# Optimization experiments

Hardware: AMD Instinct MI355X
Metric: run time of the kernel (lower is better)

## Reference

```python
import itertools
import jax, jax.numpy as jnp
import numpy as np

B, N_TOK, C = 256, 196, 512
NUM_HEADS, KEY_DIM, ATTN_RATIO, RESOLUTION = 8, 32, 4.0, 14
D_V = int(ATTN_RATIO * KEY_DIM)        # 128
DH = D_V * NUM_HEADS                   # 1024
H_QKV = DH + 2 * KEY_DIM * NUM_HEADS   # 1536
SCALE = KEY_DIM ** (-0.5)


def _build_bias_idxs(resolution):
    points = list(itertools.product(range(resolution), range(resolution)))
    attention_offsets = {}
    idxs = []
    for p1 in points:
        for p2 in points:
            offset = (abs(p1[0] - p2[0]), abs(p1[1] - p2[1]))
            if offset not in attention_offsets:
                attention_offsets[offset] = len(attention_offsets)
            idxs.append(attention_offsets[offset])
    n = len(points)
    return np.array(idxs, dtype=np.int64).reshape(n, n), len(attention_offsets)


def setup_inputs() -> dict:
    key = jax.random.key(0)
    ks = jax.random.split(key, 6)
    idxs_np, n_offsets = _build_bias_idxs(RESOLUTION)  # (196,196), 196 offsets
    return {
        "x": jax.random.normal(ks[0], (B, N_TOK, C), dtype=jnp.float32),
        "qkv_w": jax.random.normal(ks[1], (H_QKV, C), dtype=jnp.float32) * (C ** -0.5),
        "qkv_b": jax.random.normal(ks[2], (H_QKV,), dtype=jnp.float32) * 0.01,
        "proj_w": jax.random.normal(ks[3], (C, DH), dtype=jnp.float32) * (DH ** -0.5),
        "proj_b": jax.random.normal(ks[4], (C,), dtype=jnp.float32) * 0.01,
        "attention_biases": jax.random.normal(ks[5], (NUM_HEADS, n_offsets), dtype=jnp.float32) * 0.02,
        "bias_idxs": jnp.asarray(idxs_np),
    }


def reference(x, qkv_w, qkv_b, proj_w, proj_b, attention_biases, bias_idxs):
    Bsz, N, _ = x.shape
    # qkv projection: (B, N, H_QKV) -> (B, heads, N, 2*key_dim + d_v)
    qkv = x @ qkv_w.T + qkv_b
    qkv = qkv.reshape(Bsz, N, NUM_HEADS, -1).transpose(0, 2, 1, 3)
    q = qkv[..., :KEY_DIM]
    k = qkv[..., KEY_DIM:2 * KEY_DIM]
    v = qkv[..., 2 * KEY_DIM:]
    # learned relative-position bias gather: (heads, N, N)
    bias = attention_biases[:, bias_idxs]
    attn = jnp.einsum("bhnd,bhmd->bhnm", q, k) * SCALE + bias
    attn = jax.nn.softmax(attn, axis=-1)
    out = jnp.einsum("bhnm,bhmd->bhnd", attn, v)  # (B, heads, N, d_v)
    out = out.transpose(0, 2, 1, 3).reshape(Bsz, N, DH)
    return out @ proj_w.T + proj_b
```

## Files before the change

### kernel.cpp

```cpp
#include <hip/hip_runtime.h>

typedef __attribute__((ext_vector_type(8))) short bf16x8;
typedef __attribute__((ext_vector_type(4))) float f32x4;
typedef unsigned short u16;
typedef unsigned int   u32;

#define NTOK  196
#define NH    8
#define DVDIM 128
#define CDIM  512
#define DH    1024
#define SCALE2 0.25505654708103197f
#define NEG_BIG -1.0e30f
#define LOG2E 1.4426950408889634f
#define VSTRIDE 200
#define RESCALE_THR 8.0f

__device__ __forceinline__ u16 f2bf(float f) {
  u32 u = __builtin_bit_cast(u32, f);
  u32 r = u + 0x7FFFu + ((u >> 16) & 1u);
  return (u16)(r >> 16);
}

__device__ __forceinline__ u32 cvtpk(float lo, float hi) {
  u32 r;
  asm("v_cvt_pk_bf16_f32 %0, %1, %2" : "=v"(r) : "v"(lo), "v"(hi));
  return r;
}

__device__ __forceinline__ void stage16(const void* g, char* lds_wave_base, int lane) {
#if __has_builtin(__builtin_amdgcn_global_load_lds)
  __builtin_amdgcn_global_load_lds(
      (const __attribute__((address_space(1))) unsigned int*)g,
      (__attribute__((address_space(3))) unsigned int*)lds_wave_base, 16, 0, 0);
#else
  *(uint4*)(lds_wave_base + lane * 16) = *(const uint4*)g;
#endif
}

__global__ __launch_bounds__(256)
void cvt_k(const float* __restrict__ s, u16* __restrict__ d, int n8) {
  int i = blockIdx.x * 256 + threadIdx.x;
  if (i < n8) {
    const float4* sp = (const float4*)s + (size_t)i * 2;
    float4 a = sp[0], b = sp[1];
    uint4 o;
    o.x = (u32)f2bf(a.x) | ((u32)f2bf(a.y) << 16);
    o.y = (u32)f2bf(a.z) | ((u32)f2bf(a.w) << 16);
    o.z = (u32)f2bf(b.x) | ((u32)f2bf(b.y) << 16);
    o.w = (u32)f2bf(b.z) | ((u32)f2bf(b.w) << 16);
    ((uint4*)d)[i] = o;
  }
}

__global__ __launch_bounds__(224)
void biasT_k(const float* __restrict__ ab, const int* __restrict__ bidx,
             float* __restrict__ bT) {
  const int m = threadIdx.x, j = blockIdx.x, h = blockIdx.y;
  float v = NEG_BIG;
  if (j < NTOK && m < NTOK) v = ab[h * NTOK + bidx[m * NTOK + j]] * LOG2E;
  bT[((size_t)h * 256 + j) * 224 + m] = v;
}

template<int K, int NB, int EPI>
__global__ __launch_bounds__(256)
void gemm_k(const u16* __restrict__ A, const u16* __restrict__ W,
            const float* __restrict__ bias,
            u16* __restrict__ q, u16* __restrict__ kk, u16* __restrict__ vT,
            float* __restrict__ out)
{
  __shared__ __align__(16) u16 As[128 * 32];
  __shared__ __align__(16) u16 Bs[128 * 32];
  const int tid  = threadIdx.x;
  const int bid  = blockIdx.x;
  const int xcd  = bid & 7, t = bid >> 3;
  const int bn   = t % NB, bm = xcd * 49 + t / NB;
  const int lane = tid & 63, w = tid >> 6;
  const int c16  = lane & 15, quad = lane >> 4;
  const int wm   = (w >> 1) * 64, wn = (w & 1) * 64;
  f32x4 acc[4][4] = {};

  const u16* Ab = A + (size_t)bm * 128 * K;
  const u16* Wb = W + (size_t)bn * 128 * K;
  char* ldsA = (char*)As + w * 1024;
  char* ldsB = (char*)Bs + w * 1024;

  for (int k0 = 0; k0 < K; k0 += 32) {
    #pragma unroll
    for (int p = 0; p < 2; ++p) {
      const int i = p * 256 + tid;
      const int m = i >> 2, kp = (i & 3) * 8;
      stage16(Ab + (size_t)m * K + k0 + kp, ldsA + p * 4096, lane);
      stage16(Wb + (size_t)m * K + k0 + kp, ldsB + p * 4096, lane);
    }
    __syncthreads();
    bf16x8 af[4], bfr[4];
    #pragma unroll
    for (int mi = 0; mi < 4; ++mi)
      af[mi] = *(const bf16x8*)&As[(wm + mi * 16 + c16) * 32 + quad * 8];
    #pragma unroll
    for (int ni = 0; ni < 4; ++ni)
      bfr[ni] = *(const bf16x8*)&Bs[(wn + ni * 16 + c16) * 32 + quad * 8];
    #pragma unroll
    for (int mi = 0; mi < 4; ++mi)
      #pragma unroll
      for (int ni = 0; ni < 4; ++ni)
        acc[mi][ni] = __builtin_amdgcn_mfma_f32_16x16x32_bf16(af[mi], bfr[ni], acc[mi][ni], 0, 0, 0);
    __syncthreads();
  }

  if (EPI == 0) {
    #pragma unroll
    for (int ni = 0; ni < 4; ++ni) {
      const int gn = bn * 128 + wn + ni * 16 + c16;
      const int h = gn / 192, d = gn - h * 192;
      const float bv = bias[gn];
      #pragma unroll
      for (int mi = 0; mi < 4; ++mi) {
        const int gm0 = bm * 128 + wm + mi * 16 + quad * 4;
        const int bb = gm0 / 196, tok0 = gm0 - bb * 196;
        const size_t bhh = (size_t)bb * 8 + h;
        const float v0 = acc[mi][ni][0] + bv, v1 = acc[mi][ni][1] + bv;
        const float v2 = acc[mi][ni][2] + bv, v3 = acc[mi][ni][3] + bv;
        if (d < 64) {
          u16* dst = (d < 32) ? (q  + (bhh * 196 + tok0) * 32 + d)
                              : (kk + (bhh * 196 + tok0) * 32 + (d - 32));
          dst[0] = f2bf(v0); dst[32] = f2bf(v1); dst[64] = f2bf(v2); dst[96] = f2bf(v3);
        } else {
          ushort4 pk = { f2bf(v0), f2bf(v1), f2bf(v2), f2bf(v3) };
          *(ushort4*)&vT[(bhh * 128 + (d - 64)) * VSTRIDE + tok0] = pk;
        }
      }
    }
  } else {
    #pragma unroll
    for (int ni = 0; ni < 4; ++ni) {
      const int gn = bn * 128 + wn + ni * 16 + c16;
      const float bv = bias[gn];
      #pragma unroll
      for (int mi = 0; mi < 4; ++mi) {
        const int gm0 = bm * 128 + wm + mi * 16 + quad * 4;
        #pragma unroll
        for (int r = 0; r < 4; ++r)
          out[(size_t)(gm0 + r) * CDIM + gn] = acc[mi][ni][r] + bv;
      }
    }
  }
}

__global__ __launch_bounds__(256)
void attn_k(const u16* __restrict__ q, const u16* __restrict__ kk,
            const u16* __restrict__ vT, const float* __restrict__ bT,
            u16* __restrict__ Ob)
{
  __shared__ __align__(16) char smem[80896];
  u16* k_lds  = (u16*)smem;
  u16* vt_lds = (u16*)(smem + 20480);
  u16* p_lds  = (u16*)(smem + 71680);

  const int bh = blockIdx.x;
  const int b = bh >> 3, h = bh & 7;
  const int tid = threadIdx.x;
  const int lane = tid & 63, w = tid >> 6;
  const int c16 = lane & 15, quad = lane >> 4;
  const u16* qb = q  + (size_t)bh * (NTOK * 32);
  const u16* kb = kk + (size_t)bh * (NTOK * 32);
  const u16* vb = vT + (size_t)bh * (DVDIM * VSTRIDE);
  const float* bTh = bT + (size_t)h * 256 * 224;
  const f32x4 zf = {0.f, 0.f, 0.f, 0.f};
  u16* pw = p_lds + w * 16 * 72;

  {
    const char* vbb = (const char*)vb;
    for (int c = w; c < 50; c += 4)
      stage16(vbb + c * 1024 + lane * 16, (char*)vt_lds + c * 1024, lane);
  }
  #pragma unroll
  for (int p = 0; p < 4; ++p) {
    const int i = p * 256 + tid;
    const int row = i >> 2, part = (i & 3) * 8;
    const uint4 val = *(const uint4*)(kb + (size_t)min(row, NTOK - 1) * 32 + part);
    *(uint4*)&k_lds[row * 40 + part] = val;
  }
  __syncthreads();
  {
    const int row = tid >> 1, half = tid & 1;
    *(u32*)&vt_lds[row * VSTRIDE + 196 + half * 2] = 0u;
  }
  __syncthreads();

  const int nt_iter = 3 + ((w == (bh & 3)) ? 1 : 0);
  for (int t = 0; t < nt_iter; ++t) {
    const int ti = (t < 3) ? (w + 4 * t) : 12;
    const int tok = min(ti * 16 + c16, NTOK - 1);
    const bf16x8 qf = *(const bf16x8*)(qb + (size_t)tok * 32 + quad * 8);
    const int qg = min(ti * 16 + c16, 223);
    float mx = NEG_BIG, lsum = 0.f;
    f32x4 oacc[8] = {};

    for (int kc = 0; kc < 4; ++kc) {
      f32x4 sc[4];
      __builtin_amdgcn_s_setprio(1);
      #pragma unroll
      for (int nt = 0; nt < 4; ++nt) {
        bf16x8 kf = *(const bf16x8*)&k_lds[(kc * 64 + nt * 16 + c16) * 40 + quad * 8];
        sc[nt] = __builtin_amdgcn_mfma_f32_16x16x32_bf16(kf, qf, zf, 0, 0, 0);
      }
      __builtin_amdgcn_s_setprio(0);

      float ntmx[4];
      #pragma unroll
      for (int nt = 0; nt < 4; ++nt) {
        const float* bp = bTh + (size_t)(kc * 64 + nt * 16 + quad * 4) * 224 + qg;
        #pragma unroll
        for (int r = 0; r < 4; ++r)
          sc[nt][r] = sc[nt][r] * SCALE2 + bp[r * 224];
        ntmx[nt] = fmaxf(fmaxf(sc[nt][0], sc[nt][1]), fmaxf(sc[nt][2], sc[nt][3]));
      }
      const float cmx = fmaxf(fmaxf(ntmx[0], ntmx[1]), fmaxf(ntmx[2], ntmx[3]));

      float alpha = 1.0f;
      if (__ballot(cmx > mx + RESCALE_THR)) {
        float rmx = fmaxf(cmx, __shfl_xor(cmx, 16));
        rmx = fmaxf(rmx, __shfl_xor(rmx, 32));
        const float nmx = fmaxf(mx, rmx);
        alpha = exp2f(mx - nmx);
        mx = nmx;
        float a4[4];
        #pragma unroll
        for (int r = 0; r < 4; ++r) a4[r] = __shfl(alpha, quad * 4 + r);
        #pragma unroll
        for (int nt = 0; nt < 8; ++nt)
          #pragma unroll
          for (int r = 0; r < 4; ++r) oacc[nt][r] *= a4[r];
      }

      const float m = mx;
      float csum = 0.f;
      #pragma unroll
      for (int nt = 0; nt < 4; ++nt) {
        const float p0 = exp2f(sc[nt][0] - m), p1 = exp2f(sc[nt][1] - m);
        const float p2 = exp2f(sc[nt][2] - m), p3 = exp2f(sc[nt][3] - m);
        csum += (p0 + p1) + (p2 + p3);
        uint2 pk;
        pk.x = cvtpk(p0, p1);
        pk.y = cvtpk(p2, p3);
        *(uint2*)&pw[c16 * 72 + nt * 16 + quad * 4] = pk;
      }
      csum += __shfl_xor(csum, 16);
      csum += __shfl_xor(csum, 32);
      lsum = lsum * alpha + csum;

      __builtin_amdgcn_s_setprio(1);
      #pragma unroll
      for (int ks = 0; ks < 2; ++ks) {
        bf16x8 ap = *(const bf16x8*)&pw[c16 * 72 + ks * 32 + quad * 8];
        #pragma unroll
        for (int nt = 0; nt < 8; ++nt) {
          bf16x8 bv = *(const bf16x8*)&vt_lds[(nt * 16 + c16) * VSTRIDE + kc * 64 + ks * 32 + quad * 8];
          oacc[nt] = __builtin_amdgcn_mfma_f32_16x16x32_bf16(ap, bv, oacc[nt], 0, 0, 0);
        }
      }
      __builtin_amdgcn_s_setprio(0);
    }

    float lr[4];
    #pragma unroll
    for (int r = 0; r < 4; ++r) lr[r] = __shfl(lsum, quad * 4 + r);
    #pragma unroll
    for (int r = 0; r < 4; ++r) {
      const int m = ti * 16 + quad * 4 + r;
      if (m < NTOK) {
        const float inv = 1.0f / lr[r];
        #pragma unroll
        for (int nt = 0; nt < 8; ++nt)
          Ob[((size_t)b * NTOK + m) * DH + h * DVDIM + nt * 16 + c16] =
              f2bf(oacc[nt][r] * inv);
      }
    }
  }
}

extern "C" void kernel_launch(void* const* d_in, const int* in_sizes, int n_in,
                              void* d_out, int out_size, void* d_ws, size_t ws_size,
                              hipStream_t stream) {
  const float* x      = (const float*)d_in[0];
  const float* qkv_w  = (const float*)d_in[1];
  const float* qkv_b  = (const float*)d_in[2];
  const float* proj_w = (const float*)d_in[3];
  const float* proj_b = (const float*)d_in[4];
  const float* ab     = (const float*)d_in[5];
  const int*   bidx   = (const int*)d_in[6];
  float* out = (float*)d_out;

  char* p = (char*)d_ws;
  u16*   qw  = (u16*)(p);
  u16*   kw  = (u16*)(p + 25690112);
  u16*   vTw = (u16*)(p + 51380224);
  u16*   w1b = (u16*)(p + 156237824);
  u16*   w3b = (u16*)(p + 157810688);
  float* bT  = (float*)(p + 158859264);
  u16*   xb  = (u16*)(p + 160694272);
  u16*   Ob  = (u16*)(p + 160694272);

  cvt_k<<<12544, 256, 0, stream>>>(x,      xb,  3211264);
  cvt_k<<<  384, 256, 0, stream>>>(qkv_w,  w1b,   98304);
  cvt_k<<<  256, 256, 0, stream>>>(proj_w, w3b,   65536);
  biasT_k<<<dim3(256, 8), 224, 0, stream>>>(ab, bidx, bT);

  gemm_k<512, 12, 0><<<4704, 256, 0, stream>>>(xb, w1b, qkv_b, qw, kw, vTw, nullptr);

  attn_k<<<2048, 256, 0, stream>>>(qw, kw, vTw, bT, Ob);

  gemm_k<1024, 4, 1><<<1568, 256, 0, stream>>>(Ob, w3b, proj_b, nullptr, nullptr, nullptr, out);
}
```

Before: 541.6 us.

## Read V directly from global memory instead of staging it in LDS

The attention kernel no longer copies the transposed V tile into shared memory. The PV MFMA loop now loads V fragments straight from global memory, and zeroing of V's padding columns moves into the QKV projection epilogue. Shared memory per block shrinks from about 80KB to about 25KB, which is meant to allow more resident blocks per CU and remove the staging pass and a barrier. In exchange, each wave re-reads V through the cache hierarchy for every query tile, adding load latency inside the hot loop, and the last head may read slightly past the end of the buffer.

```diff
diff --git a/kernel.cpp b/kernel.cpp
--- a/kernel.cpp
+++ b/kernel.cpp
@@ -128,7 +128,12 @@
           dst[0] = f2bf(v0); dst[32] = f2bf(v1); dst[64] = f2bf(v2); dst[96] = f2bf(v3);
         } else {
           ushort4 pk = { f2bf(v0), f2bf(v1), f2bf(v2), f2bf(v3) };
-          *(ushort4*)&vT[(bhh * 128 + (d - 64)) * VSTRIDE + tok0] = pk;
+          u16* vrow = vT + (bhh * 128 + (d - 64)) * VSTRIDE;
+          *(ushort4*)&vrow[tok0] = pk;
+          if (tok0 == 192) {
+            ushort4 z = {0, 0, 0, 0};
+            *(ushort4*)&vrow[196] = z;
+          }
         }
       }
     }
@@ -153,10 +158,9 @@
             const u16* __restrict__ vT, const float* __restrict__ bT,
             u16* __restrict__ Ob)
 {
-  __shared__ __align__(16) char smem[80896];
-  u16* k_lds  = (u16*)smem;
-  u16* vt_lds = (u16*)(smem + 20480);
-  u16* p_lds  = (u16*)(smem + 71680);
+  __shared__ __align__(16) char smem[25216];
+  u16* k_lds = (u16*)smem;
+  u16* p_lds = (u16*)(smem + 16000);
 
   const int bh = blockIdx.x;
   const int b = bh >> 3, h = bh & 7;
@@ -170,22 +174,10 @@
   const f32x4 zf = {0.f, 0.f, 0.f, 0.f};
   u16* pw = p_lds + w * 16 * 72;
 
-  {
-    const char* vbb = (const char*)vb;
-    for (int c = w; c < 50; c += 4)
-      stage16(vbb + c * 1024 + lane * 16, (char*)vt_lds + c * 1024, lane);
-  }
-  #pragma unroll
-  for (int p = 0; p < 4; ++p) {
-    const int i = p * 256 + tid;
+  for (int i = tid; i < 800; i += 256) {
     const int row = i >> 2, part = (i & 3) * 8;
-    const uint4 val = *(const uint4*)(kb + (size_t)min(row, NTOK - 1) * 32 + part);
-    *(uint4*)&k_lds[row * 40 + part] = val;
-  }
-  __syncthreads();
-  {
-    const int row = tid >> 1, half = tid & 1;
-    *(u32*)&vt_lds[row * VSTRIDE + 196 + half * 2] = 0u;
+    *(uint4*)&k_lds[row * 40 + part] =
+        *(const uint4*)(kb + (size_t)min(row, NTOK - 1) * 32 + part);
   }
   __syncthreads();
 
@@ -203,7 +195,8 @@
       __builtin_amdgcn_s_setprio(1);
       #pragma unroll
       for (int nt = 0; nt < 4; ++nt) {
-        bf16x8 kf = *(const bf16x8*)&k_lds[(kc * 64 + nt * 16 + c16) * 40 + quad * 8];
+        const int krow = min(kc * 64 + nt * 16 + c16, 199);
+        bf16x8 kf = *(const bf16x8*)&k_lds[krow * 40 + quad * 8];
         sc[nt] = __builtin_amdgcn_mfma_f32_16x16x32_bf16(kf, qf, zf, 0, 0, 0);
       }
       __builtin_amdgcn_s_setprio(0);
@@ -257,7 +250,8 @@
         bf16x8 ap = *(const bf16x8*)&pw[c16 * 72 + ks * 32 + quad * 8];
         #pragma unroll
         for (int nt = 0; nt < 8; ++nt) {
-          bf16x8 bv = *(const bf16x8*)&vt_lds[(nt * 16 + c16) * VSTRIDE + kc * 64 + ks * 32 + quad * 8];
+          bf16x8 bv = *(const bf16x8*)(vb + (size_t)(nt * 16 + c16) * VSTRIDE
+                                          + kc * 64 + ks * 32 + quad * 8);
           oacc[nt] = __builtin_amdgcn_mfma_f32_16x16x32_bf16(ap, bv, oacc[nt], 0, 0, 0);
         }
       }
```

Result: slower. 646.4 us (+19.4%).
